# Performance work log

Measured on AMD Instinct MI355X. Metric: run time of the kernel, lower is better.

The kernel has to match this reference:

```python
import jax, jax.numpy as jnp
import numpy as np

BETA = 0.25


def setup_inputs() -> dict:
    key = jax.random.key(0)
    k1, k2 = jax.random.split(key)
    x = jax.random.normal(k1, (64, 32, 32, 64), dtype=jnp.float32)
    # codebook stored as [embedding_dim, num_embeddings], as in the layer
    embeddings = jax.random.normal(k2, (64, 1024), dtype=jnp.float32) * 0.05
    return {"x": x, "embeddings": embeddings}


def reference(x, embeddings):
    input_shape = x.shape
    d = embeddings.shape[0]
    flat = x.reshape(-1, d)  # [N, D]

    sim = flat @ embeddings  # [N, K]
    distances = (
        jnp.sum(flat ** 2, axis=1, keepdims=True)
        + jnp.sum(embeddings ** 2, axis=0)
        - 2.0 * sim
    )
    encoding_indices = jnp.argmin(distances, axis=1)  # [N]

    # one_hot @ embeddings.T is mathematically a gather of codebook rows
    quantized = jnp.take(embeddings.T, encoding_indices, axis=0)  # [N, D]
    quantized = quantized.reshape(input_shape)

    commitment_loss = jnp.mean((jax.lax.stop_gradient(quantized) - x) ** 2)
    codebook_loss = jnp.mean((quantized - jax.lax.stop_gradient(x)) ** 2)
    loss = BETA * commitment_loss + codebook_loss

    # straight-through estimator
    quantized_st = x + jax.lax.stop_gradient(quantized - x)
    return quantized_st, loss
```

## Files before the change

### kernel.cpp

```cpp
#include <hip/hip_runtime.h>

#define D 64
#define K 1024
#define NPTS 65536
#define OUT_ELEMS (NPTS * D)
#define PAD4 17

typedef _Float16 f16x8 __attribute__((ext_vector_type(8)));
typedef float    f32x4 __attribute__((ext_vector_type(4)));

#define SCL  4096.0f
#define ISCL 0.000244140625f


static __device__ __forceinline__ void split16(float v, _Float16& h, _Float16& ls) {
    h = (_Float16)v;
    const float r = (v - (float)h) * SCL;
    ls = (_Float16)r;
}

__global__ __launch_bounds__(256) void vq_prep(const float* __restrict__ emb,
                                               float* __restrict__ eT,
                                               float* __restrict__ enorm_h,
                                               _Float16* __restrict__ eh,
                                               _Float16* __restrict__ els,
                                               float* __restrict__ loss_out) {
    __shared__ float tile[64][65];
    const int t    = threadIdx.x;
    const int lane = t & 63;
    const int quad = t >> 6;
    const int k0   = blockIdx.x * 64;

#pragma unroll
    for (int i = 0; i < 16; ++i) {
        const int d = i * 4 + quad;
        tile[d][lane] = emb[d * K + k0 + lane];
    }
    __syncthreads();

    const int kk = t >> 2, c = t & 3;
    const int krow = k0 + kk;
#pragma unroll
    for (int j = 0; j < 16; ++j) {
        const int d = c * 16 + j;
        const float v = tile[d][kk];
        const int idx = krow * D + d;
        eT[idx] = v;
        _Float16 h, ls;
        split16(v, h, ls);
        eh[idx] = h; els[idx] = ls;
    }

    if (t < 64) {
        float s = __fmul_rn(tile[0][t], tile[0][t]);
        for (int dd = 1; dd < D; ++dd)
            s = __fadd_rn(s, __fmul_rn(tile[dd][t], tile[dd][t]));
        enorm_h[k0 + t] = 0.5f * s;
    }
    if (blockIdx.x == 0 && t == 0) *loss_out = 0.0f;
}

static __device__ __forceinline__ float sq8(float a, float b, float c, float d,
                                            float e, float f, float g, float h) {
    float r = __fmul_rn(a, a);
    r = __fadd_rn(r, __fmul_rn(b, b));
    r = __fadd_rn(r, __fmul_rn(c, c));
    r = __fadd_rn(r, __fmul_rn(d, d));
    r = __fadd_rn(r, __fmul_rn(e, e));
    r = __fadd_rn(r, __fmul_rn(f, f));
    r = __fadd_rn(r, __fmul_rn(g, g));
    r = __fadd_rn(r, __fmul_rn(h, h));
    return r;
}

#define PINF(v) asm volatile("" : "+v"(v))

#define MFMA(A, B, C) C = __builtin_amdgcn_mfma_f32_16x16x32_f16(A, B, C, 0, 0, 0)

#define MKFRAG16(FH, FS, U0, U1) {                        \
    _Float16 h_, s_;                                      \
    split16(U0.x, h_, s_); FH[0]=h_; FS[0]=s_;            \
    split16(U0.y, h_, s_); FH[1]=h_; FS[1]=s_;            \
    split16(U0.z, h_, s_); FH[2]=h_; FS[2]=s_;            \
    split16(U0.w, h_, s_); FH[3]=h_; FS[3]=s_;            \
    split16(U1.x, h_, s_); FH[4]=h_; FS[4]=s_;            \
    split16(U1.y, h_, s_); FH[5]=h_; FS[5]=s_;            \
    split16(U1.z, h_, s_); FH[6]=h_; FS[6]=s_;            \
    split16(U1.w, h_, s_); FH[7]=h_; FS[7]=s_; }

static __device__ __forceinline__ void cp16(const void* gptr, void* lptr) {
    __builtin_amdgcn_global_load_lds(
        (const __attribute__((address_space(1))) void*)gptr,
        (__attribute__((address_space(3))) void*)lptr, 16, 0, 0);
}

__global__ __launch_bounds__(512, 4) void vq_main(const float* __restrict__ x,
        const float* __restrict__ eT, const float* __restrict__ enorm_h,
        const _Float16* __restrict__ eh, const _Float16* __restrict__ els,
        float* __restrict__ out, float* __restrict__ loss_out) {
    __shared__ __align__(16) char smem[55808];
    float*  rpart = (float*)(smem + 16384);
    int*    swin  = (int*)(smem + 20480);
    float*  skey  = (float*)(smem + 20992);
    int*    sct   = (int*)(smem + 37376);
    float4* slab  = (float4*)(smem + 20992);

    const int t     = threadIdx.x;
    const int lane  = t & 63;
    const int w     = t >> 6;
    const int m     = lane & 15;
    const int quad  = lane >> 4;
    const int g     = w >> 1;
    const int h     = w & 1;
    const int pbase = blockIdx.x * 128 + g * 32;

    const int n0   = lane >> 3;
    const int jj   = lane & 7;
    const int soff = n0 * 128 + (((jj - n0) & 7) << 4);
    const int hs   = w >> 2;
    const char* gsrc = ((w >> 1) & 1) ? (const char*)els : (const char*)eh;
    const char* gsb  = gsrc + (w & 1) * 1024 + soff;
    const int   dA   = hs * 4096 + ((w >> 1) & 1) * 2048 + (w & 1) * 1024;

    const int o0 = (m * 8 + ((quad + m) & 7)) * 16;
    const int o1 = (m * 8 + ((4 + quad + m) & 7)) * 16;

    cp16(gsb + (size_t)(hs * 32) * 2048, smem + dA);

    f16x8 Ah00, As00, Ah01, As01;
    f16x8 Ah10, As10, Ah11, As11;
#define LOADA(TT, HH, FH, FS) {                                            \
    const float* px = x + ((size_t)(pbase + TT * 16 + m)) * D + HH * 32 + quad * 8; \
    const float4 u0 = *(const float4*)px;                                  \
    const float4 u1 = *(const float4*)(px + 4);                            \
    if (h == 0)                                                            \
        rpart[(g * 32 + TT * 16 + m) * 8 + (HH * 4 + quad)] =              \
            sq8(u0.x, u0.y, u0.z, u0.w, u1.x, u1.y, u1.z, u1.w);           \
    MKFRAG16(FH, FS, u0, u1); }
    LOADA(0, 0, Ah00, As00)
    LOADA(0, 1, Ah01, As01)
    LOADA(1, 0, Ah10, As10)
    LOADA(1, 1, Ah11, As11)
#undef LOADA
    PINF(Ah00); PINF(As00); PINF(Ah01); PINF(As01);
    PINF(Ah10); PINF(As10); PINF(Ah11); PINF(As11);

    const float FINF = 3.402823466e38f;
    float bk00 = FINF, bk01 = FINF, bk02 = FINF, bk03 = FINF;
    float bk10 = FINF, bk11 = FINF, bk12 = FINF, bk13 = FINF;
    int   bc00 = 0, bc01 = 0, bc02 = 0, bc03 = 0;
    int   bc10 = 0, bc11 = 0, bc12 = 0, bc13 = 0;

#define TILE_BODY(BBOFF, CT, PRET, PREOFF) {                               \
    __syncthreads();     \
    cp16(gsb + (size_t)(hs * 32 + (PRET)) * 2048, smem + (PREOFF) + dA);   \
    const char* bb = smem + (BBOFF) + h * 4096;                            \
    const f16x8 Bh0 = *(const f16x8*)(bb + o0);                            \
    const f16x8 Bh1 = *(const f16x8*)(bb + o1);                            \
    const f16x8 Bs0 = *(const f16x8*)(bb + 2048 + o0);                     \
    const f16x8 Bs1 = *(const f16x8*)(bb + 2048 + o1);                     \
    const float enh = enorm_h[h * 512 + (CT) * 16 + m];                    \
    f32x4 m0a = {0.f,0.f,0.f,0.f}, m0b = {0.f,0.f,0.f,0.f};                \
    f32x4 c0a = {0.f,0.f,0.f,0.f}, c0b = {0.f,0.f,0.f,0.f};                \
    f32x4 m1a = {0.f,0.f,0.f,0.f}, m1b = {0.f,0.f,0.f,0.f};                \
    f32x4 c1a = {0.f,0.f,0.f,0.f}, c1b = {0.f,0.f,0.f,0.f};                \
    MFMA(Ah00, Bh0, m0a); MFMA(Ah10, Bh0, m1a);           \
    MFMA(Ah01, Bh1, m0b); MFMA(Ah11, Bh1, m1b);           \
    MFMA(As00, Bh0, c0a); MFMA(As10, Bh0, c1a);                \
    MFMA(As01, Bh1, c0b); MFMA(As11, Bh1, c1b);                            \
    MFMA(Ah00, Bs0, c0a); MFMA(Ah10, Bs0, c1a);                \
    MFMA(Ah01, Bs1, c0b); MFMA(Ah11, Bs1, c1b);                            \
    const f32x4 d0 = (m0a + m0b) + ISCL * (c0a + c0b);                     \
    const f32x4 d1 = (m1a + m1b) + ISCL * (c1a + c1b);                     \
    { const float kv = enh - d0[0]; if (kv < bk00) { bk00 = kv; bc00 = (CT); } } \
    { const float kv = enh - d0[1]; if (kv < bk01) { bk01 = kv; bc01 = (CT); } } \
    { const float kv = enh - d0[2]; if (kv < bk02) { bk02 = kv; bc02 = (CT); } } \
    { const float kv = enh - d0[3]; if (kv < bk03) { bk03 = kv; bc03 = (CT); } } \
    { const float kv = enh - d1[0]; if (kv < bk10) { bk10 = kv; bc10 = (CT); } } \
    { const float kv = enh - d1[1]; if (kv < bk11) { bk11 = kv; bc11 = (CT); } } \
    { const float kv = enh - d1[2]; if (kv < bk12) { bk12 = kv; bc12 = (CT); } } \
    { const float kv = enh - d1[3]; if (kv < bk13) { bk13 = kv; bc13 = (CT); } } }

    for (int j = 0; j < 16; ++j) {
        const int ct0 = 2 * j;
        const int ct1 = 2 * j + 1;
        const int tp2 = (2 * j + 2) & 31;
        TILE_BODY(0,    ct0, ct1, 8192)
        TILE_BODY(8192, ct1, tp2, 0)
    }
#undef TILE_BODY

#define PUTC(TT, REG, BK, BC) {                                   \
    const int ploc = g * 32 + TT * 16 + quad * 4 + REG;           \
    skey[ploc * 32 + h * 16 + m] = BK;                            \
    sct [ploc * 32 + h * 16 + m] = BC; }
    PUTC(0, 0, bk00, bc00) PUTC(0, 1, bk01, bc01)
    PUTC(0, 2, bk02, bc02) PUTC(0, 3, bk03, bc03)
    PUTC(1, 0, bk10, bc10) PUTC(1, 1, bk11, bc11)
    PUTC(1, 2, bk12, bc12) PUTC(1, 3, bk13, bc13)
#undef PUTC
    __syncthreads();

    if (t < 128) {
        const int p = t;
        const float* rp = rpart + p * 8;
        const float A = ((rp[0] + rp[1]) + (rp[2] + rp[3])) +
                        ((rp[4] + rp[5]) + (rp[6] + rp[7]));
        float fb = FINF;
        int   fi = 0;
#pragma unroll
        for (int c = 0; c < 32; ++c) {
            const float kv = skey[p * 32 + c];
            const int   iv = (c >> 4) * 512 + sct[p * 32 + c] * 16 + (c & 15);
            if (kv < fb || (kv == fb && iv < fi)) { fb = kv; fi = iv; }
        }
        swin[p] = fi;
        float lp = fmaf(2.0f, fb, A);
#pragma unroll
        for (int off = 32; off > 0; off >>= 1) lp += __shfl_down(lp, off, 64);
        if (lane == 0) atomicAdd(loss_out, lp * (1.25f / (float)OUT_ELEMS));
    }
    __syncthreads();

    {
        const int p = t >> 2, c = t & 3;
        const int fi = swin[p];
        const float4* qr = (const float4*)(eT + (size_t)fi * D) + c * 4;
        float4* dst = slab + p * PAD4 + c * 4;
#pragma unroll
        for (int j = 0; j < 4; ++j) dst[j] = qr[j];
    }
    __syncthreads();
    float4* og = (float4*)out + (size_t)blockIdx.x * 2048;
#pragma unroll
    for (int s = 0; s < 4; ++s) {
        const int f = s * 512 + t;
        og[f] = slab[(f >> 4) * PAD4 + (f & 15)];
    }
}

extern "C" void kernel_launch(void* const* d_in, const int* in_sizes, int n_in,
                              void* d_out, int out_size, void* d_ws, size_t ws_size,
                              hipStream_t stream) {
    const float* x   = (const float*)d_in[0];
    const float* emb = (const float*)d_in[1];
    float* out       = (float*)d_out;
    char*  ws        = (char*)d_ws;
    float*    eT      = (float*)ws;
    float*    enorm_h = (float*)(ws + 262144);
    _Float16* eh      = (_Float16*)(ws + 266240);
    _Float16* els     = (_Float16*)(ws + 397312);
    float* loss_out   = out + OUT_ELEMS;

    vq_prep<<<dim3(K / 64), dim3(256), 0, stream>>>(emb, eT, enorm_h, eh, els,
                                                    loss_out);
    vq_main<<<dim3(NPTS / 128), dim3(512), 0, stream>>>(x, eT, enorm_h, eh,
                                                        els, out, loss_out);
}
```

Measured before the change: 112.3 us.

## Pre-swizzle codebook into MFMA fragment layout and read B operands directly from global

The prep kernel now writes the f16 hi/lo codebook halves in an MFMA-fragment-major layout, so each lane can load its B fragments straight from global/L2 with contiguous 16-byte reads. This removes the LDS double-buffered async copy and the per-tile __syncthreads. The final gather writes directly from eT to the output instead of staging through an LDS slab, and the key/index scratch arrays get a 33-element padded stride to reduce LDS bank conflicts. LDS use drops, but every wave re-reads the codebook through the cache hierarchy, which adds global load latency to the MFMA loop.

```diff
diff --git a/kernel.cpp b/kernel.cpp
--- a/kernel.cpp
+++ b/kernel.cpp
@@ -4,7 +4,6 @@
 #define K 1024
 #define NPTS 65536
 #define OUT_ELEMS (NPTS * D)
-#define PAD4 17
 
 typedef _Float16 f16x8 __attribute__((ext_vector_type(8)));
 typedef float    f32x4 __attribute__((ext_vector_type(4)));
@@ -22,8 +21,8 @@
 __global__ __launch_bounds__(256) void vq_prep(const float* __restrict__ emb,
                                                float* __restrict__ eT,
                                                float* __restrict__ enorm_h,
-                                               _Float16* __restrict__ eh,
-                                               _Float16* __restrict__ els,
+                                               _Float16* __restrict__ ehf,
+                                               _Float16* __restrict__ elf,
                                                float* __restrict__ loss_out) {
     __shared__ float tile[64][65];
     const int t    = threadIdx.x;
@@ -40,15 +39,17 @@
 
     const int kk = t >> 2, c = t & 3;
     const int krow = k0 + kk;
+    const int ct   = krow >> 4, col = krow & 15;
 #pragma unroll
     for (int j = 0; j < 16; ++j) {
         const int d = c * 16 + j;
         const float v = tile[d][kk];
-        const int idx = krow * D + d;
-        eT[idx] = v;
+        eT[krow * D + d] = v;
         _Float16 h, ls;
         split16(v, h, ls);
-        eh[idx] = h; els[idx] = ls;
+        const int off = ((ct * 2 + (d >> 5)) * 64 + ((d >> 3) & 3) * 16 + col) * 8
+                        + (d & 7);
+        ehf[off] = h; elf[off] = ls;
     }
 
     if (t < 64) {
@@ -88,22 +89,15 @@
     split16(U1.z, h_, s_); FH[6]=h_; FS[6]=s_;            \
     split16(U1.w, h_, s_); FH[7]=h_; FS[7]=s_; }
 
-static __device__ __forceinline__ void cp16(const void* gptr, void* lptr) {
-    __builtin_amdgcn_global_load_lds(
-        (const __attribute__((address_space(1))) void*)gptr,
-        (__attribute__((address_space(3))) void*)lptr, 16, 0, 0);
-}
-
 __global__ __launch_bounds__(512, 4) void vq_main(const float* __restrict__ x,
         const float* __restrict__ eT, const float* __restrict__ enorm_h,
-        const _Float16* __restrict__ eh, const _Float16* __restrict__ els,
+        const _Float16* __restrict__ ehf, const _Float16* __restrict__ elf,
         float* __restrict__ out, float* __restrict__ loss_out) {
-    __shared__ __align__(16) char smem[55808];
-    float*  rpart = (float*)(smem + 16384);
-    int*    swin  = (int*)(smem + 20480);
-    float*  skey  = (float*)(smem + 20992);
-    int*    sct   = (int*)(smem + 37376);
-    float4* slab  = (float4*)(smem + 20992);
+    __shared__ __align__(16) char smem[38400];
+    float* rpart = (float*)smem;
+    int*   swin  = (int*)(smem + 4096);
+    float* skey  = (float*)(smem + 4608);
+    int*   sct   = (int*)(smem + 21504);
 
     const int t     = threadIdx.x;
     const int lane  = t & 63;
@@ -113,19 +107,6 @@
     const int g     = w >> 1;
     const int h     = w & 1;
     const int pbase = blockIdx.x * 128 + g * 32;
-
-    const int n0   = lane >> 3;
-    const int jj   = lane & 7;
-    const int soff = n0 * 128 + (((jj - n0) & 7) << 4);
-    const int hs   = w >> 2;
-    const char* gsrc = ((w >> 1) & 1) ? (const char*)els : (const char*)eh;
-    const char* gsb  = gsrc + (w & 1) * 1024 + soff;
-    const int   dA   = hs * 4096 + ((w >> 1) & 1) * 2048 + (w & 1) * 1024;
-
-    const int o0 = (m * 8 + ((quad + m) & 7)) * 16;
-    const int o1 = (m * 8 + ((4 + quad + m) & 7)) * 16;
-
-    cp16(gsb + (size_t)(hs * 32) * 2048, smem + dA);
 
     f16x8 Ah00, As00, Ah01, As01;
     f16x8 Ah10, As10, Ah11, As11;
@@ -151,49 +132,45 @@
     int   bc00 = 0, bc01 = 0, bc02 = 0, bc03 = 0;
     int   bc10 = 0, bc11 = 0, bc12 = 0, bc13 = 0;
 
-#define TILE_BODY(BBOFF, CT, PRET, PREOFF) {                               \
-    __syncthreads();     \
-    cp16(gsb + (size_t)(hs * 32 + (PRET)) * 2048, smem + (PREOFF) + dA);   \
-    const char* bb = smem + (BBOFF) + h * 4096;                            \
-    const f16x8 Bh0 = *(const f16x8*)(bb + o0);                            \
-    const f16x8 Bh1 = *(const f16x8*)(bb + o1);                            \
-    const f16x8 Bs0 = *(const f16x8*)(bb + 2048 + o0);                     \
-    const f16x8 Bs1 = *(const f16x8*)(bb + 2048 + o1);                     \
-    const float enh = enorm_h[h * 512 + (CT) * 16 + m];                    \
-    f32x4 m0a = {0.f,0.f,0.f,0.f}, m0b = {0.f,0.f,0.f,0.f};                \
-    f32x4 c0a = {0.f,0.f,0.f,0.f}, c0b = {0.f,0.f,0.f,0.f};                \
-    f32x4 m1a = {0.f,0.f,0.f,0.f}, m1b = {0.f,0.f,0.f,0.f};                \
-    f32x4 c1a = {0.f,0.f,0.f,0.f}, c1b = {0.f,0.f,0.f,0.f};                \
-    MFMA(Ah00, Bh0, m0a); MFMA(Ah10, Bh0, m1a);           \
-    MFMA(Ah01, Bh1, m0b); MFMA(Ah11, Bh1, m1b);           \
-    MFMA(As00, Bh0, c0a); MFMA(As10, Bh0, c1a);                \
-    MFMA(As01, Bh1, c0b); MFMA(As11, Bh1, c1b);                            \
-    MFMA(Ah00, Bs0, c0a); MFMA(Ah10, Bs0, c1a);                \
-    MFMA(Ah01, Bs1, c0b); MFMA(Ah11, Bs1, c1b);                            \
-    const f32x4 d0 = (m0a + m0b) + ISCL * (c0a + c0b);                     \
-    const f32x4 d1 = (m1a + m1b) + ISCL * (c1a + c1b);                     \
-    { const float kv = enh - d0[0]; if (kv < bk00) { bk00 = kv; bc00 = (CT); } } \
-    { const float kv = enh - d0[1]; if (kv < bk01) { bk01 = kv; bc01 = (CT); } } \
-    { const float kv = enh - d0[2]; if (kv < bk02) { bk02 = kv; bc02 = (CT); } } \
-    { const float kv = enh - d0[3]; if (kv < bk03) { bk03 = kv; bc03 = (CT); } } \
-    { const float kv = enh - d1[0]; if (kv < bk10) { bk10 = kv; bc10 = (CT); } } \
-    { const float kv = enh - d1[1]; if (kv < bk11) { bk11 = kv; bc11 = (CT); } } \
-    { const float kv = enh - d1[2]; if (kv < bk12) { bk12 = kv; bc12 = (CT); } } \
-    { const float kv = enh - d1[3]; if (kv < bk13) { bk13 = kv; bc13 = (CT); } } }
-
-    for (int j = 0; j < 16; ++j) {
-        const int ct0 = 2 * j;
-        const int ct1 = 2 * j + 1;
-        const int tp2 = (2 * j + 2) & 31;
-        TILE_BODY(0,    ct0, ct1, 8192)
-        TILE_BODY(8192, ct1, tp2, 0)
-    }
-#undef TILE_BODY
+    const _Float16* bhp = ehf + (size_t)h * 32768 + (size_t)lane * 8;
+    const _Float16* bsp = elf + (size_t)h * 32768 + (size_t)lane * 8;
+    const float*    enp = enorm_h + h * 512 + m;
+
+#pragma unroll 2
+    for (int tt = 0; tt < 32; ++tt) {
+        const f16x8 Bh0 = *(const f16x8*)(bhp);
+        const f16x8 Bh1 = *(const f16x8*)(bhp + 512);
+        const f16x8 Bs0 = *(const f16x8*)(bsp);
+        const f16x8 Bs1 = *(const f16x8*)(bsp + 512);
+        bhp += 1024; bsp += 1024;
+        const float enh = enp[tt * 16];
+
+        f32x4 m0a = {0.f,0.f,0.f,0.f}, m0b = {0.f,0.f,0.f,0.f};
+        f32x4 c0a = {0.f,0.f,0.f,0.f}, c0b = {0.f,0.f,0.f,0.f};
+        f32x4 m1a = {0.f,0.f,0.f,0.f}, m1b = {0.f,0.f,0.f,0.f};
+        f32x4 c1a = {0.f,0.f,0.f,0.f}, c1b = {0.f,0.f,0.f,0.f};
+        MFMA(Ah00, Bh0, m0a); MFMA(Ah10, Bh0, m1a);
+        MFMA(Ah01, Bh1, m0b); MFMA(Ah11, Bh1, m1b);
+        MFMA(As00, Bh0, c0a); MFMA(As10, Bh0, c1a);
+        MFMA(As01, Bh1, c0b); MFMA(As11, Bh1, c1b);
+        MFMA(Ah00, Bs0, c0a); MFMA(Ah10, Bs0, c1a);
+        MFMA(Ah01, Bs1, c0b); MFMA(Ah11, Bs1, c1b);
+        const f32x4 d0 = (m0a + m0b) + ISCL * (c0a + c0b);
+        const f32x4 d1 = (m1a + m1b) + ISCL * (c1a + c1b);
+        { const float kv = enh - d0[0]; if (kv < bk00) { bk00 = kv; bc00 = tt; } }
+        { const float kv = enh - d0[1]; if (kv < bk01) { bk01 = kv; bc01 = tt; } }
+        { const float kv = enh - d0[2]; if (kv < bk02) { bk02 = kv; bc02 = tt; } }
+        { const float kv = enh - d0[3]; if (kv < bk03) { bk03 = kv; bc03 = tt; } }
+        { const float kv = enh - d1[0]; if (kv < bk10) { bk10 = kv; bc10 = tt; } }
+        { const float kv = enh - d1[1]; if (kv < bk11) { bk11 = kv; bc11 = tt; } }
+        { const float kv = enh - d1[2]; if (kv < bk12) { bk12 = kv; bc12 = tt; } }
+        { const float kv = enh - d1[3]; if (kv < bk13) { bk13 = kv; bc13 = tt; } }
+    }
 
 #define PUTC(TT, REG, BK, BC) {                                   \
     const int ploc = g * 32 + TT * 16 + quad * 4 + REG;           \
-    skey[ploc * 32 + h * 16 + m] = BK;                            \
-    sct [ploc * 32 + h * 16 + m] = BC; }
+    skey[ploc * 33 + h * 16 + m] = BK;                            \
+    sct [ploc * 33 + h * 16 + m] = BC; }
     PUTC(0, 0, bk00, bc00) PUTC(0, 1, bk01, bc01)
     PUTC(0, 2, bk02, bc02) PUTC(0, 3, bk03, bc03)
     PUTC(1, 0, bk10, bc10) PUTC(1, 1, bk11, bc11)
@@ -210,8 +187,8 @@
         int   fi = 0;
 #pragma unroll
         for (int c = 0; c < 32; ++c) {
-            const float kv = skey[p * 32 + c];
-            const int   iv = (c >> 4) * 512 + sct[p * 32 + c] * 16 + (c & 15);
+            const float kv = skey[p * 33 + c];
+            const int   iv = (c >> 4) * 512 + sct[p * 33 + c] * 16 + (c & 15);
             if (kv < fb || (kv == fb && iv < fi)) { fb = kv; fi = iv; }
         }
         swin[p] = fi;
@@ -223,19 +200,14 @@
     __syncthreads();
 
     {
-        const int p = t >> 2, c = t & 3;
-        const int fi = swin[p];
-        const float4* qr = (const float4*)(eT + (size_t)fi * D) + c * 4;
-        float4* dst = slab + p * PAD4 + c * 4;
-#pragma unroll
-        for (int j = 0; j < 4; ++j) dst[j] = qr[j];
-    }
-    __syncthreads();
-    float4* og = (float4*)out + (size_t)blockIdx.x * 2048;
-#pragma unroll
-    for (int s = 0; s < 4; ++s) {
-        const int f = s * 512 + t;
-        og[f] = slab[(f >> 4) * PAD4 + (f & 15)];
+        const float4* eT4 = (const float4*)eT;
+        float4* og = (float4*)out + (size_t)blockIdx.x * 2048;
+#pragma unroll
+        for (int s = 0; s < 4; ++s) {
+            const int f  = s * 512 + t;
+            const int fi = swin[f >> 4];
+            og[f] = eT4[(size_t)fi * 16 + (f & 15)];
+        }
     }
 }
 
@@ -248,12 +220,12 @@
     char*  ws        = (char*)d_ws;
     float*    eT      = (float*)ws;
     float*    enorm_h = (float*)(ws + 262144);
-    _Float16* eh      = (_Float16*)(ws + 266240);
-    _Float16* els     = (_Float16*)(ws + 397312);
+    _Float16* ehf     = (_Float16*)(ws + 266240);
+    _Float16* elf     = (_Float16*)(ws + 397312);
     float* loss_out   = out + OUT_ELEMS;
 
-    vq_prep<<<dim3(K / 64), dim3(256), 0, stream>>>(emb, eT, enorm_h, eh, els,
+    vq_prep<<<dim3(K / 64), dim3(256), 0, stream>>>(emb, eT, enorm_h, ehf, elf,
                                                     loss_out);
-    vq_main<<<dim3(NPTS / 128), dim3(512), 0, stream>>>(x, eT, enorm_h, eh,
-                                                        els, out, loss_out);
-}
+    vq_main<<<dim3(NPTS / 128), dim3(512), 0, stream>>>(x, eT, enorm_h, ehf,
+                                                        elf, out, loss_out);
+}
```

After: 115.4 us. +2.8%, slower.
